# Performance work log

Measured on AMD Instinct MI355X. Metric: run time of the kernel, lower is better.

## Reference

```python
import jax, jax.numpy as jnp
import numpy as np

B, P1, P2 = 32, 25, 24          # batch, patch rows (+1 cls row), patch cols
D1, D2, D3 = 8, 8, 12           # factored embed dims (total d = 768)
H1, H2, H3 = 2, 2, 4            # factored heads (16 total)
X, Y, Z = D1 // H1, D2 // H2, D3 // H3   # per-head factor dims -> head dim 48
SCALE = float((X * Y * Z) ** -0.5)


def tle(x, w1, w2, w3, b):
    # Tensor Linear Embedding: mode-wise linear maps on the last 3 modes + bias.
    return jnp.einsum('bpqijk,ai,cj,dk->bpqacd', x, w1, w2, w3) + b


def split_heads(t):
    # (b,p1,p2,(x h1),(y h2),(z h3)) -> (b,h1,h2,h3, p1*p2, x*y*z)
    b, p1, p2, _, _, _ = t.shape
    t = t.reshape(b, p1, p2, X, H1, Y, H2, Z, H3)
    t = t.transpose(0, 4, 6, 8, 1, 2, 3, 5, 7)
    return t.reshape(b, H1, H2, H3, p1 * p2, X * Y * Z)


def merge_heads(t, p1, p2):
    # (b,h1,h2,h3,S,D) -> (b,p1,p2,(x h1),(y h2),(z h3))
    b = t.shape[0]
    t = t.reshape(b, H1, H2, H3, p1, p2, X, Y, Z)
    t = t.transpose(0, 4, 5, 6, 1, 7, 2, 8, 3)
    return t.reshape(b, p1, p2, X * H1, Y * H2, Z * H3)


def setup_inputs() -> dict:
    key = jax.random.key(0)
    ks = jax.random.split(key, 20)

    def w(k, shape):
        return jax.random.normal(k, shape, jnp.float32) * 0.02

    inp = {"x": jax.random.normal(ks[0], (B, P1, P2, D1, D2, D3), jnp.float32)}
    for i, n in enumerate(["q", "k", "v", "o"]):
        inp[f"w{n}1"] = w(ks[1 + 4 * i], (D1, D1))
        inp[f"w{n}2"] = w(ks[2 + 4 * i], (D2, D2))
        inp[f"w{n}3"] = w(ks[3 + 4 * i], (D3, D3))
        inp[f"b{n}"] = w(ks[4 + 4 * i], (D1, D2, D3))
    return inp


def reference(x, wq1, wq2, wq3, bq, wk1, wk2, wk3, bk,
              wv1, wv2, wv3, bv, wo1, wo2, wo3, bo):
    q = split_heads(tle(x, wq1, wq2, wq3, bq))
    k = split_heads(tle(x, wk1, wk2, wk3, bk))
    v = split_heads(tle(x, wv1, wv2, wv3, bv))
    # scores: (b,h1,h2,h3,S,S) with S = 600
    attn = jax.nn.softmax(jnp.einsum('befgsd,befgtd->befgst', q, k) * SCALE, axis=-1)
    o = jnp.einsum('befgst,befgtd->befgsd', attn, v)
    o = merge_heads(o, P1, P2)
    return tle(o, wo1, wo2, wo3, bo)
```

## Files before the change

### kernel.cpp

```cpp
#include <hip/hip_runtime.h>
#include <hip/hip_bf16.h>
#include <cstdint>

#define Bc    32
#define Sc    600
#define NHc   16
#define SP    640
#define NKT   19
#define DHc   48
#define DP    64
#define QW    48
#define SCALEc 0.14433756729740643f

typedef __bf16   bf16x8 __attribute__((ext_vector_type(8)));
typedef float    f32x4  __attribute__((ext_vector_type(4)));
typedef float    f32x16 __attribute__((ext_vector_type(16)));
typedef uint32_t u32x4  __attribute__((ext_vector_type(4)));

static __device__ __forceinline__ f32x16 mfma32(bf16x8 a, bf16x8 b, f32x16 c) {
    return __builtin_amdgcn_mfma_f32_32x32x16_bf16(a, b, c, 0, 0, 0);
}
static __device__ __forceinline__ unsigned short f2bf(float f) {
    uint32_t u = __builtin_bit_cast(uint32_t, f);
    u += 0x7FFFu + ((u >> 16) & 1u);
    return (unsigned short)(u >> 16);
}
static __device__ __forceinline__ float bfbits(uint32_t w, int odd) {
    return __builtin_bit_cast(float, odd ? (w & 0xffff0000u) : (w << 16));
}
static __device__ __forceinline__ f32x16 fzero16() {
    f32x16 z;
    #pragma unroll
    for (int i = 0; i < 16; ++i) z[i] = 0.f;
    return z;
}
static __device__ __forceinline__ void gload_lds16(const void* g, void* l) {
    __builtin_amdgcn_global_load_lds(
        (const __attribute__((address_space(1))) unsigned int*)g,
        (__attribute__((address_space(3))) unsigned int*)l, 16, 0, 0);
}

__global__ __launch_bounds__(256) void tle_qkv(
    const float* __restrict__ x,
    const float* __restrict__ wq1, const float* __restrict__ wq2,
    const float* __restrict__ wq3, const float* __restrict__ bq,
    const float* __restrict__ wk1, const float* __restrict__ wk2,
    const float* __restrict__ wk3, const float* __restrict__ bk,
    const float* __restrict__ wv1, const float* __restrict__ wv2,
    const float* __restrict__ wv3, const float* __restrict__ bv,
    __hip_bfloat16* __restrict__ Qb, __hip_bfloat16* __restrict__ Kb,
    __hip_bfloat16* __restrict__ Vr)
{
    __shared__ __align__(16) unsigned short t1s[3][4][8][104];
    __shared__ __align__(16) char uni[4*3*16*48*2];
    float (*xs)[768] = (float(*)[768])uni;
    typedef unsigned short outrow_t[3][16][48];
    outrow_t* outs = (outrow_t*)uni;

    const int t = threadIdx.x;
    const int p = t >> 6, a = (t >> 3) & 7, c = t & 7;
    const int patch0 = blockIdx.x * 4;

    {
        const float4* xg = (const float4*)(x + (size_t)patch0 * 768);
        float4* xl = (float4*)uni;
        xl[t] = xg[t]; xl[t + 256] = xg[t + 256]; xl[t + 512] = xg[t + 512];
    }
    float w1r[3][8], w2r[3][8];
    #pragma unroll
    for (int pr = 0; pr < 3; ++pr) {
        const float* w1 = pr == 0 ? wq1 : pr == 1 ? wk1 : wv1;
        const float* w2 = pr == 0 ? wq2 : pr == 1 ? wk2 : wv2;
        #pragma unroll
        for (int i = 0; i < 8; ++i) { w1r[pr][i] = w1[a*8 + i]; w2r[pr][i] = w2[c*8 + i]; }
    }
    __syncthreads();

    float s1[3][12];
    #pragma unroll
    for (int pr = 0; pr < 3; ++pr)
        #pragma unroll
        for (int k = 0; k < 12; ++k) s1[pr][k] = 0.f;
    #pragma unroll
    for (int i = 0; i < 8; ++i) {
        const float4* xr = (const float4*)&xs[p][i*96 + c*12];
        float4 v0 = xr[0], v1 = xr[1], v2 = xr[2];
        #pragma unroll
        for (int pr = 0; pr < 3; ++pr) {
            float wv = w1r[pr][i];
            s1[pr][0] += wv*v0.x; s1[pr][1] += wv*v0.y; s1[pr][2]  += wv*v0.z; s1[pr][3]  += wv*v0.w;
            s1[pr][4] += wv*v1.x; s1[pr][5] += wv*v1.y; s1[pr][6]  += wv*v1.z; s1[pr][7]  += wv*v1.w;
            s1[pr][8] += wv*v2.x; s1[pr][9] += wv*v2.y; s1[pr][10] += wv*v2.z; s1[pr][11] += wv*v2.w;
        }
    }
    #pragma unroll
    for (int pr = 0; pr < 3; ++pr) {
        uint32_t pk[6];
        #pragma unroll
        for (int n = 0; n < 6; ++n)
            asm("v_cvt_pk_bf16_f32 %0, %1, %2" : "=v"(pk[n])
                : "v"(s1[pr][2*n]), "v"(s1[pr][2*n+1]));
        unsigned short* row = &t1s[pr][p][a][0];
        *(uint2*)(row + c*12 + 0) = make_uint2(pk[0], pk[1]);
        *(uint2*)(row + c*12 + 4) = make_uint2(pk[2], pk[3]);
        *(uint2*)(row + c*12 + 8) = make_uint2(pk[4], pk[5]);
    }
    __syncthreads();

    #pragma unroll
    for (int pr = 0; pr < 3; ++pr) {
        uint4 q[12];
        const uint4* t1p = (const uint4*)&t1s[pr][p][a][0];
        #pragma unroll
        for (int n = 0; n < 12; ++n) q[n] = t1p[n];
        float t2r[12];
        #pragma unroll
        for (int k = 0; k < 12; ++k) t2r[k] = 0.f;
        #pragma unroll
        for (int j = 0; j < 8; ++j) {
            float wv = w2r[pr][j];
            #pragma unroll
            for (int k = 0; k < 12; ++k) {
                int idx = j*12 + k;
                uint32_t ww = __builtin_bit_cast(u32x4, q[idx >> 3])[(idx >> 1) & 3];
                t2r[k] += wv * bfbits(ww, idx & 1);
            }
        }
        const float* w3p = pr == 0 ? wq3 : pr == 1 ? wk3 : wv3;
        const float* bb  = pr == 0 ? bq  : pr == 1 ? bk  : bv;
        const float4* bp = (const float4*)(bb + a*96 + c*12);
        float4 b0 = bp[0], b1 = bp[1], b2 = bp[2];
        float bias_[12] = {b0.x,b0.y,b0.z,b0.w, b1.x,b1.y,b1.z,b1.w, b2.x,b2.y,b2.z,b2.w};
        #pragma unroll
        for (int d = 0; d < 12; ++d) {
            const float4* wr = (const float4*)(w3p + d*12);
            float4 u0 = wr[0], u1 = wr[1], u2 = wr[2];
            float od = bias_[d]
                + t2r[0]*u0.x + t2r[1]*u0.y + t2r[2] *u0.z + t2r[3] *u0.w
                + t2r[4]*u1.x + t2r[5]*u1.y + t2r[6] *u1.z + t2r[7] *u1.w
                + t2r[8]*u2.x + t2r[9]*u2.y + t2r[10]*u2.z + t2r[11]*u2.w;
            if (pr == 0) od *= SCALEc;
            int h  = (a & 1)*8 + (c & 1)*4 + (d & 3);
            int dh = (a >> 1)*12 + (c >> 1)*3 + (d >> 2);
            outs[p][pr][h][dh] = f2bf(od);
        }
    }
    __syncthreads();

    #pragma unroll 1
    for (int u = t; u < 1152; u += 256) {
        int pr = u / 384, r = u - pr*384;
        int pp = r / 96,  r2 = r - pp*96;
        int h = r2 / 6,   u6 = r2 - h*6;
        uint4 v = *(const uint4*)&outs[pp][pr][h][u6*8];
        int patch = patch0 + pp;
        int b = patch / Sc, s = patch - b * Sc;
        if (pr == 0)
            *(uint4*)(Qb + ((size_t)(b*NHc + h) * SP + s) * QW + u6*8) = v;
        else if (pr == 1)
            *(uint4*)(Kb + ((size_t)(b*NHc + h) * SP + s) * DP + u6*8) = v;
        else
            *(uint4*)(Vr + ((size_t)(b*NHc + h) * SP + s) * DP + u6*8) = v;
    }
}

__global__ __launch_bounds__(256) void vtrans(
    const __hip_bfloat16* __restrict__ Vr, __hip_bfloat16* __restrict__ Vt,
    __hip_bfloat16* __restrict__ Kb)
{
    __shared__ __align__(16) short Ls[64][72];
    const int t = threadIdx.x;
    const int bh = blockIdx.x, st = blockIdx.y;
    const __hip_bfloat16* src = Vr + ((size_t)bh * SP + st*64) * DP;
    for (int u = t; u < 512; u += 256) {
        int r = u >> 3, c = (u & 7) * 8;
        *(bf16x8*)&Ls[r][c] = *(const bf16x8*)(src + (size_t)r * DP + c);
    }
    __syncthreads();
    const unsigned short one_bf = 0x3F80;
    for (int u = t; u < 384; u += 256) {
        int dh = u >> 3, cb = (u & 7) * 8;
        int gcol = st*64 + cb;
        if (gcol >= Sc + 8) continue;
        union { unsigned short s[8]; bf16x8 v; } o;
        if (gcol >= Sc) {
            #pragma unroll
            for (int j = 0; j < 8; ++j) o.s[j] = 0;
        } else {
            #pragma unroll
            for (int j = 0; j < 8; ++j) o.s[j] = (unsigned short)Ls[cb + j][dh];
        }
        *(bf16x8*)(Vt + ((size_t)bh*64 + dh) * SP + st*64 + cb) = o.v;
    }
    if (t < 128) {
        int r = 48 + (t >> 3), cb = (t & 7) * 8;
        union { unsigned short s[8]; bf16x8 v; } o;
        #pragma unroll
        for (int j = 0; j < 8; ++j) {
            int col = st*64 + cb + j;
            o.s[j] = (r == 48 && col < Sc) ? one_bf : (unsigned short)0;
        }
        *(bf16x8*)(Vt + ((size_t)bh*64 + r) * SP + st*64 + cb) = o.v;
    }
    if (st == 9 && t < 64) {
        int r = 600 + (t >> 3), cb = (t & 7) * 8;
        union { unsigned short s[8]; bf16x8 v; } z;
        #pragma unroll
        for (int j = 0; j < 8; ++j) z.s[j] = 0;
        *(bf16x8*)(Kb + ((size_t)bh * SP + r) * DP + cb) = z.v;
    }
}

static __device__ __forceinline__ void softmax_pack(
    const f32x16& sv, bf16x8& pf0, bf16x8& pf1)
{
    float p[16];
    #pragma unroll
    for (int r = 0; r < 16; ++r) p[r] = __expf(sv[r]);
    uint32_t Wa0, Wa1, Wa2, Wa3, Wb0, Wb1, Wb2, Wb3;
    asm("v_cvt_pk_bf16_f32 %0, %1, %2" : "=v"(Wa0) : "v"(p[0]),  "v"(p[1]));
    asm("v_cvt_pk_bf16_f32 %0, %1, %2" : "=v"(Wb0) : "v"(p[2]),  "v"(p[3]));
    asm("v_cvt_pk_bf16_f32 %0, %1, %2" : "=v"(Wa1) : "v"(p[4]),  "v"(p[5]));
    asm("v_cvt_pk_bf16_f32 %0, %1, %2" : "=v"(Wb1) : "v"(p[6]),  "v"(p[7]));
    asm("v_cvt_pk_bf16_f32 %0, %1, %2" : "=v"(Wa2) : "v"(p[8]),  "v"(p[9]));
    asm("v_cvt_pk_bf16_f32 %0, %1, %2" : "=v"(Wb2) : "v"(p[10]), "v"(p[11]));
    asm("v_cvt_pk_bf16_f32 %0, %1, %2" : "=v"(Wa3) : "v"(p[12]), "v"(p[13]));
    asm("v_cvt_pk_bf16_f32 %0, %1, %2" : "=v"(Wb3) : "v"(p[14]), "v"(p[15]));
    asm("v_permlane32_swap_b32 %0, %1" : "+v"(Wa0), "+v"(Wa1));
    asm("v_permlane32_swap_b32 %0, %1" : "+v"(Wb0), "+v"(Wb1));
    asm("v_permlane32_swap_b32 %0, %1" : "+v"(Wa2), "+v"(Wa3));
    asm("v_permlane32_swap_b32 %0, %1" : "+v"(Wb2), "+v"(Wb3));
    pf0 = __builtin_bit_cast(bf16x8, (u32x4){Wa0, Wb0, Wa1, Wb1});
    pf1 = __builtin_bit_cast(bf16x8, (u32x4){Wa2, Wb2, Wa3, Wb3});
}

__global__ __launch_bounds__(64, 2) void attn_mfma(
    const __hip_bfloat16* __restrict__ Qb, const __hip_bfloat16* __restrict__ Kb,
    const __hip_bfloat16* __restrict__ Vt, float* __restrict__ Ob)
{
    __shared__ __align__(16) char Ks[2][4096];
    __shared__ __align__(16) char Vs[2][4096];
    const int l = threadIdx.x;
    const int q32 = l & 31, hl = l >> 5;
    const int bid = blockIdx.x;
    const int lg = (bid & 7) * 320 + (bid >> 3);
    const int bh = lg / 5, qb = lg - bh * 5;
    const int b = bh >> 4, h = bh & 15;

    const char* Kbh = (const char*)(Kb + (size_t)bh * SP * DP);
    const char* Vbh = (const char*)(Vt + (size_t)bh * 64 * SP);

    const int krow = l >> 3;
    const char* ksrc = Kbh + krow*128 + (((l & 7)*16) ^ (krow << 4));
    const char* vsrc = Vbh + (size_t)(l >> 2)*(SP*2) + (l & 3)*16;

    bf16x8 qf[4][3];
    #pragma unroll
    for (int f = 0; f < 4; ++f) {
        const __hip_bfloat16* Qp = Qb + ((size_t)bh*SP + qb*128 + f*32 + q32) * QW;
        #pragma unroll
        for (int ck = 0; ck < 3; ++ck)
            qf[f][ck] = *(const bf16x8*)(Qp + ck*16 + hl*8);
    }
    f32x16 acc[4][2];
    #pragma unroll
    for (int f = 0; f < 4; ++f) { acc[f][0] = fzero16(); acc[f][1] = fzero16(); }

    auto stage = [&](int kt, int bfi) {
        const char* ks = ksrc + (size_t)kt * 4096;
        const char* vs = vsrc + (size_t)kt * 64;
        #pragma unroll
        for (int i = 0; i < 4; ++i)
            gload_lds16(ks + i*1024, &Ks[bfi][i*1024]);
        #pragma unroll
        for (int i = 0; i < 4; ++i)
            gload_lds16(vs + (size_t)i*16*(SP*2), &Vs[bfi][i*1024]);
    };

    stage(0, 0);
    int bfi = 0;
    #pragma unroll 1
    for (int kt = 0; kt < NKT; ++kt) {
        asm volatile("s_waitcnt vmcnt(0)" ::: "memory");
        __builtin_amdgcn_sched_barrier(0);
        bf16x8 kf[3], vf[2][2];
        #pragma unroll
        for (int ck = 0; ck < 3; ++ck)
            kf[ck] = *(const bf16x8*)&Ks[bfi][q32*128 + ((ck*32 + hl*16) ^ ((q32 & 7) << 4))];
        #pragma unroll
        for (int db = 0; db < 2; ++db)
            #pragma unroll
            for (int c2 = 0; c2 < 2; ++c2)
                vf[db][c2] = *(const bf16x8*)&Vs[bfi][(db*32 + q32)*64 + c2*32 + hl*16];
        if (kt + 1 < NKT) stage(kt + 1, bfi ^ 1);
        __builtin_amdgcn_s_setprio(1);
        #pragma unroll
        for (int f = 0; f < 4; ++f) {
            f32x16 s = fzero16();
            s = mfma32(kf[0], qf[f][0], s);
            s = mfma32(kf[1], qf[f][1], s);
            s = mfma32(kf[2], qf[f][2], s);
            bf16x8 pf0, pf1;
            softmax_pack(s, pf0, pf1);
            acc[f][0] = mfma32(vf[0][0], pf0, acc[f][0]);
            acc[f][0] = mfma32(vf[0][1], pf1, acc[f][0]);
            acc[f][1] = mfma32(vf[1][0], pf0, acc[f][1]);
            acc[f][1] = mfma32(vf[1][1], pf1, acc[f][1]);
        }
        __builtin_amdgcn_s_setprio(0);
        bfi ^= 1;
    }

    #pragma unroll
    for (int f = 0; f < 4; ++f) {
        float ls = acc[f][1][8];
        float other = __shfl_xor(ls, 32);
        float tot = hl ? other : ls;
        float inv = 1.f / tot;
        int q = qb*128 + f*32 + q32;
        if (q < Sc) {
            float* orow = Ob + ((size_t)b*Sc + q)*768 + h*48;
            #pragma unroll
            for (int rq = 0; rq < 4; ++rq) {
                int d0 = rq*8 + hl*4;
                float4 v4 = make_float4(acc[f][0][rq*4+0]*inv, acc[f][0][rq*4+1]*inv,
                                        acc[f][0][rq*4+2]*inv, acc[f][0][rq*4+3]*inv);
                *(float4*)(orow + d0) = v4;
            }
            #pragma unroll
            for (int rq = 0; rq < 2; ++rq) {
                int d0 = 32 + rq*8 + hl*4;
                float4 v4 = make_float4(acc[f][1][rq*4+0]*inv, acc[f][1][rq*4+1]*inv,
                                        acc[f][1][rq*4+2]*inv, acc[f][1][rq*4+3]*inv);
                *(float4*)(orow + d0) = v4;
            }
        }
    }
}

__global__ __launch_bounds__(256) void tle_out(
    const float* __restrict__ Oin, const float* __restrict__ w1g,
    const float* __restrict__ w2g, const float* __restrict__ w3g,
    const float* __restrict__ bias, float* __restrict__ out)
{
    __shared__ __align__(16) float xs[4][768];
    __shared__ __align__(16) unsigned short t1s[4][8][104];
    const int t = threadIdx.x;
    const int p = t >> 6, a = (t >> 3) & 7, c = t & 7;
    const int lane = t & 63;
    const int patch = blockIdx.x * 4 + p;
    for (int o4 = lane; o4 < 192; o4 += 64) {
        float4 v = *(const float4*)(Oin + (size_t)patch * 768 + o4*4);
        int h = o4 / 12, r = o4 - h*12;
        #pragma unroll
        for (int q = 0; q < 4; ++q) {
            int dh = r*4 + q;
            int xq = dh / 12, rem2 = dh - xq*12, yq = rem2 / 3, zq = rem2 - yq*3;
            int aa = xq*2 + (h >> 3), cc = yq*2 + ((h >> 2) & 1), dd = zq*4 + (h & 3);
            xs[p][aa*96 + cc*12 + dd] = ((const float*)&v)[q];
        }
    }
    float w1r[8], w2r[8];
    #pragma unroll
    for (int i = 0; i < 8; ++i) { w1r[i] = w1g[a*8 + i]; w2r[i] = w2g[c*8 + i]; }
    __syncthreads();

    float s1[12];
    #pragma unroll
    for (int k = 0; k < 12; ++k) s1[k] = 0.f;
    #pragma unroll
    for (int i = 0; i < 8; ++i) {
        const float4* xr = (const float4*)&xs[p][i*96 + c*12];
        float4 v0 = xr[0], v1 = xr[1], v2 = xr[2];
        float wv = w1r[i];
        s1[0] += wv*v0.x; s1[1] += wv*v0.y; s1[2]  += wv*v0.z; s1[3]  += wv*v0.w;
        s1[4] += wv*v1.x; s1[5] += wv*v1.y; s1[6]  += wv*v1.z; s1[7]  += wv*v1.w;
        s1[8] += wv*v2.x; s1[9] += wv*v2.y; s1[10] += wv*v2.z; s1[11] += wv*v2.w;
    }
    {
        uint32_t pk[6];
        #pragma unroll
        for (int n = 0; n < 6; ++n)
            asm("v_cvt_pk_bf16_f32 %0, %1, %2" : "=v"(pk[n])
                : "v"(s1[2*n]), "v"(s1[2*n+1]));
        unsigned short* row = &t1s[p][a][0];
        *(uint2*)(row + c*12 + 0) = make_uint2(pk[0], pk[1]);
        *(uint2*)(row + c*12 + 4) = make_uint2(pk[2], pk[3]);
        *(uint2*)(row + c*12 + 8) = make_uint2(pk[4], pk[5]);
    }
    __syncthreads();

    uint4 q[12];
    const uint4* t1p = (const uint4*)&t1s[p][a][0];
    #pragma unroll
    for (int n = 0; n < 12; ++n) q[n] = t1p[n];
    float t2r[12];
    #pragma unroll
    for (int k = 0; k < 12; ++k) t2r[k] = 0.f;
    #pragma unroll
    for (int j = 0; j < 8; ++j) {
        float wv = w2r[j];
        #pragma unroll
        for (int k = 0; k < 12; ++k) {
            int idx = j*12 + k;
            uint32_t ww = __builtin_bit_cast(u32x4, q[idx >> 3])[(idx >> 1) & 3];
            t2r[k] += wv * bfbits(ww, idx & 1);
        }
    }
    const float4* bp = (const float4*)(bias + a*96 + c*12);
    float4 b0 = bp[0], b1 = bp[1], b2 = bp[2];
    float bias_[12] = {b0.x,b0.y,b0.z,b0.w, b1.x,b1.y,b1.z,b1.w, b2.x,b2.y,b2.z,b2.w};
    float od[12];
    #pragma unroll
    for (int d = 0; d < 12; ++d) {
        const float4* wr = (const float4*)(w3g + d*12);
        float4 u0 = wr[0], u1 = wr[1], u2 = wr[2];
        od[d] = bias_[d]
            + t2r[0]*u0.x + t2r[1]*u0.y + t2r[2] *u0.z + t2r[3] *u0.w
            + t2r[4]*u1.x + t2r[5]*u1.y + t2r[6] *u1.z + t2r[7] *u1.w
            + t2r[8]*u2.x + t2r[9]*u2.y + t2r[10]*u2.z + t2r[11]*u2.w;
    }
    float4* op = (float4*)(out + (size_t)patch*768 + a*96 + c*12);
    op[0] = make_float4(od[0], od[1], od[2],  od[3]);
    op[1] = make_float4(od[4], od[5], od[6],  od[7]);
    op[2] = make_float4(od[8], od[9], od[10], od[11]);
}

extern "C" void kernel_launch(void* const* d_in, const int* in_sizes, int n_in,
                              void* d_out, int out_size, void* d_ws, size_t ws_size,
                              hipStream_t stream) {
    const float* x   = (const float*)d_in[0];
    const float* wq1 = (const float*)d_in[1];
    const float* wq2 = (const float*)d_in[2];
    const float* wq3 = (const float*)d_in[3];
    const float* bq  = (const float*)d_in[4];
    const float* wk1 = (const float*)d_in[5];
    const float* wk2 = (const float*)d_in[6];
    const float* wk3 = (const float*)d_in[7];
    const float* bk  = (const float*)d_in[8];
    const float* wv1 = (const float*)d_in[9];
    const float* wv2 = (const float*)d_in[10];
    const float* wv3 = (const float*)d_in[11];
    const float* bv  = (const float*)d_in[12];
    const float* wo1 = (const float*)d_in[13];
    const float* wo2 = (const float*)d_in[14];
    const float* wo3 = (const float*)d_in[15];
    const float* bo  = (const float*)d_in[16];
    float* out = (float*)d_out;

    char* ws = (char*)d_ws;
    const size_t SZ_Q = (size_t)512 * SP * QW * 2;
    const size_t SZ_K = (size_t)512 * SP * DP * 2;
    __hip_bfloat16* Qb = (__hip_bfloat16*)ws;
    __hip_bfloat16* Kb = (__hip_bfloat16*)(ws + SZ_Q);
    __hip_bfloat16* Vr = (__hip_bfloat16*)(ws + SZ_Q + SZ_K);
    __hip_bfloat16* Vt = (__hip_bfloat16*)(ws + SZ_Q + 2*SZ_K);
    float*          Ob = (float*)(ws + SZ_Q + 3*SZ_K);

    dim3 blk(256);
    tle_qkv<<<Bc*Sc/4, blk, 0, stream>>>(x, wq1, wq2, wq3, bq,
                                         wk1, wk2, wk3, bk,
                                         wv1, wv2, wv3, bv, Qb, Kb, Vr);
    vtrans<<<dim3(512, 10), blk, 0, stream>>>(Vr, Vt, Kb);
    attn_mfma<<<2560, 64, 0, stream>>>(Qb, Kb, Vt, Ob);
    tle_out<<<Bc*Sc/4, blk, 0, stream>>>(Ob, wo1, wo2, wo3, bo, out);
}
```

Baseline: 178.6 us.

## Rewrite QKV tensor embedding with MFMA Kronecker-factored first stage and fp16 dot2

The QKV projection kernel now processes 16 patches per block. The first two mode products are fused into one GEMM by forming the Kronecker product of w1 and w2 in bf16 and running it on 16x16x32 MFMA instructions. The third mode uses packed fp16 dot2 instructions on an fp16 intermediate held in LDS, and each thread writes one full contiguous head row directly to global memory. This replaces scalar FMA loops and a separate LDS transpose-and-store pass, at the cost of lower intermediate precision (bf16 weights product, fp16 intermediate) and a serial loop over the three projections with barriers.

```diff
diff --git a/kernel.cpp b/kernel.cpp
--- a/kernel.cpp
+++ b/kernel.cpp
@@ -12,21 +12,21 @@
 #define QW    48
 #define SCALEc 0.14433756729740643f
 
-typedef __bf16   bf16x8 __attribute__((ext_vector_type(8)));
-typedef float    f32x4  __attribute__((ext_vector_type(4)));
-typedef float    f32x16 __attribute__((ext_vector_type(16)));
-typedef uint32_t u32x4  __attribute__((ext_vector_type(4)));
-
+typedef __bf16    bf16x8 __attribute__((ext_vector_type(8)));
+typedef float     f32x4  __attribute__((ext_vector_type(4)));
+typedef float     f32x16 __attribute__((ext_vector_type(16)));
+typedef uint32_t  u32x4  __attribute__((ext_vector_type(4)));
+typedef _Float16  f16x2  __attribute__((ext_vector_type(2)));
+
+static __device__ __forceinline__ f32x4 mfma16(bf16x8 a, bf16x8 b, f32x4 c) {
+    return __builtin_amdgcn_mfma_f32_16x16x32_bf16(a, b, c, 0, 0, 0);
+}
 static __device__ __forceinline__ f32x16 mfma32(bf16x8 a, bf16x8 b, f32x16 c) {
     return __builtin_amdgcn_mfma_f32_32x32x16_bf16(a, b, c, 0, 0, 0);
 }
-static __device__ __forceinline__ unsigned short f2bf(float f) {
-    uint32_t u = __builtin_bit_cast(uint32_t, f);
-    u += 0x7FFFu + ((u >> 16) & 1u);
-    return (unsigned short)(u >> 16);
-}
-static __device__ __forceinline__ float bfbits(uint32_t w, int odd) {
-    return __builtin_bit_cast(float, odd ? (w & 0xffff0000u) : (w << 16));
+static __device__ __forceinline__ float fdot2u(uint32_t a, uint32_t b, float c) {
+    return __builtin_amdgcn_fdot2(__builtin_bit_cast(f16x2, a),
+                                  __builtin_bit_cast(f16x2, b), c, false);
 }
 static __device__ __forceinline__ f32x16 fzero16() {
     f32x16 z;
@@ -40,7 +40,7 @@
         (__attribute__((address_space(3))) unsigned int*)l, 16, 0, 0);
 }
 
-__global__ __launch_bounds__(256) void tle_qkv(
+__global__ __launch_bounds__(256, 3) void tle_qkv(
     const float* __restrict__ x,
     const float* __restrict__ wq1, const float* __restrict__ wq2,
     const float* __restrict__ wq3, const float* __restrict__ bq,
@@ -51,116 +51,150 @@
     __hip_bfloat16* __restrict__ Qb, __hip_bfloat16* __restrict__ Kb,
     __hip_bfloat16* __restrict__ Vr)
 {
-    __shared__ __align__(16) unsigned short t1s[3][4][8][104];
-    __shared__ __align__(16) char uni[4*3*16*48*2];
-    float (*xs)[768] = (float(*)[768])uni;
-    typedef unsigned short outrow_t[3][16][48];
-    outrow_t* outs = (outrow_t*)uni;
-
+    __shared__ __align__(16) unsigned short xb[16*864];
+    __shared__ __align__(16) unsigned short t2s[16*776];
     const int t = threadIdx.x;
-    const int p = t >> 6, a = (t >> 3) & 7, c = t & 7;
-    const int patch0 = blockIdx.x * 4;
+    const int patch0 = blockIdx.x * 16;
 
     {
-        const float4* xg = (const float4*)(x + (size_t)patch0 * 768);
-        float4* xl = (float4*)uni;
-        xl[t] = xg[t]; xl[t + 256] = xg[t + 256]; xl[t + 512] = xg[t + 512];
-    }
-    float w1r[3][8], w2r[3][8];
-    #pragma unroll
+        const int pl = t >> 4, ij0 = (t & 15) * 4;
+        const float4* xg = (const float4*)(x + (size_t)(patch0 + pl) * 768 + ij0*12);
+        float vv[4][12];
+        #pragma unroll
+        for (int ij = 0; ij < 4; ++ij) {
+            float4 a = xg[ij*3+0], b = xg[ij*3+1], c = xg[ij*3+2];
+            vv[ij][0]=a.x; vv[ij][1]=a.y; vv[ij][2]=a.z;  vv[ij][3]=a.w;
+            vv[ij][4]=b.x; vv[ij][5]=b.y; vv[ij][6]=b.z;  vv[ij][7]=b.w;
+            vv[ij][8]=c.x; vv[ij][9]=c.y; vv[ij][10]=c.z; vv[ij][11]=c.w;
+        }
+        #pragma unroll
+        for (int k = 0; k < 12; ++k) {
+            uint32_t lo, hi;
+            asm("v_cvt_pk_bf16_f32 %0, %1, %2" : "=v"(lo) : "v"(vv[0][k]), "v"(vv[1][k]));
+            asm("v_cvt_pk_bf16_f32 %0, %1, %2" : "=v"(hi) : "v"(vv[2][k]), "v"(vv[3][k]));
+            *(uint2*)&xb[pl*864 + k*72 + ij0] = make_uint2(lo, hi);
+        }
+    }
+    __syncthreads();
+
+    const int l = t & 63, w = t >> 6;
+    const int r16 = l & 15, g = l >> 4;
+
+    bf16x8 Bf[3][2];
+    int pl_c[3], k_c[3];
+    #pragma unroll
+    for (int n = 0; n < 3; ++n) {
+        int col = n*16 + r16;
+        int pp = col / 12, kk = col - pp*12;
+        pl_c[n] = w*4 + pp; k_c[n] = kk;
+        #pragma unroll
+        for (int kh = 0; kh < 2; ++kh)
+            Bf[n][kh] = *(const bf16x8*)&xb[pl_c[n]*864 + kk*72 + kh*32 + g*8];
+    }
+
+    const int plo = t >> 4, h = t & 15;
+    const int h1 = h >> 3, h2 = (h >> 2) & 1, h3 = h & 3;
+    const int patch3 = patch0 + plo;
+    const int b3 = patch3 / Sc, s3 = patch3 - b3*Sc;
+
+    #pragma unroll 1
     for (int pr = 0; pr < 3; ++pr) {
         const float* w1 = pr == 0 ? wq1 : pr == 1 ? wk1 : wv1;
         const float* w2 = pr == 0 ? wq2 : pr == 1 ? wk2 : wv2;
-        #pragma unroll
-        for (int i = 0; i < 8; ++i) { w1r[pr][i] = w1[a*8 + i]; w2r[pr][i] = w2[c*8 + i]; }
-    }
-    __syncthreads();
-
-    float s1[3][12];
-    #pragma unroll
-    for (int pr = 0; pr < 3; ++pr)
-        #pragma unroll
-        for (int k = 0; k < 12; ++k) s1[pr][k] = 0.f;
-    #pragma unroll
-    for (int i = 0; i < 8; ++i) {
-        const float4* xr = (const float4*)&xs[p][i*96 + c*12];
-        float4 v0 = xr[0], v1 = xr[1], v2 = xr[2];
-        #pragma unroll
-        for (int pr = 0; pr < 3; ++pr) {
-            float wv = w1r[pr][i];
-            s1[pr][0] += wv*v0.x; s1[pr][1] += wv*v0.y; s1[pr][2]  += wv*v0.z; s1[pr][3]  += wv*v0.w;
-            s1[pr][4] += wv*v1.x; s1[pr][5] += wv*v1.y; s1[pr][6]  += wv*v1.z; s1[pr][7]  += wv*v1.w;
-            s1[pr][8] += wv*v2.x; s1[pr][9] += wv*v2.y; s1[pr][10] += wv*v2.z; s1[pr][11] += wv*v2.w;
-        }
-    }
-    #pragma unroll
-    for (int pr = 0; pr < 3; ++pr) {
-        uint32_t pk[6];
-        #pragma unroll
-        for (int n = 0; n < 6; ++n)
-            asm("v_cvt_pk_bf16_f32 %0, %1, %2" : "=v"(pk[n])
-                : "v"(s1[pr][2*n]), "v"(s1[pr][2*n+1]));
-        unsigned short* row = &t1s[pr][p][a][0];
-        *(uint2*)(row + c*12 + 0) = make_uint2(pk[0], pk[1]);
-        *(uint2*)(row + c*12 + 4) = make_uint2(pk[2], pk[3]);
-        *(uint2*)(row + c*12 + 8) = make_uint2(pk[4], pk[5]);
-    }
-    __syncthreads();
-
-    #pragma unroll
-    for (int pr = 0; pr < 3; ++pr) {
-        uint4 q[12];
-        const uint4* t1p = (const uint4*)&t1s[pr][p][a][0];
-        #pragma unroll
-        for (int n = 0; n < 12; ++n) q[n] = t1p[n];
-        float t2r[12];
-        #pragma unroll
-        for (int k = 0; k < 12; ++k) t2r[k] = 0.f;
-        #pragma unroll
-        for (int j = 0; j < 8; ++j) {
-            float wv = w2r[pr][j];
-            #pragma unroll
-            for (int k = 0; k < 12; ++k) {
-                int idx = j*12 + k;
-                uint32_t ww = __builtin_bit_cast(u32x4, q[idx >> 3])[(idx >> 1) & 3];
-                t2r[k] += wv * bfbits(ww, idx & 1);
+        float w2r[8];
+        #pragma unroll
+        for (int j = 0; j < 8; ++j) w2r[j] = w2[(r16 & 7)*8 + j];
+        bf16x8 Af[4][2];
+        #pragma unroll
+        for (int m = 0; m < 4; ++m) {
+            int a = 2*m + (r16 >> 3);
+            #pragma unroll
+            for (int kh = 0; kh < 2; ++kh) {
+                float w1v = w1[a*8 + kh*4 + g];
+                uint32_t wd[4];
+                #pragma unroll
+                for (int q = 0; q < 4; ++q)
+                    asm("v_cvt_pk_bf16_f32 %0, %1, %2" : "=v"(wd[q])
+                        : "v"(w1v*w2r[2*q]), "v"(w1v*w2r[2*q+1]));
+                Af[m][kh] = __builtin_bit_cast(bf16x8, (u32x4){wd[0],wd[1],wd[2],wd[3]});
             }
         }
-        const float* w3p = pr == 0 ? wq3 : pr == 1 ? wk3 : wv3;
-        const float* bb  = pr == 0 ? bq  : pr == 1 ? bk  : bv;
-        const float4* bp = (const float4*)(bb + a*96 + c*12);
-        float4 b0 = bp[0], b1 = bp[1], b2 = bp[2];
-        float bias_[12] = {b0.x,b0.y,b0.z,b0.w, b1.x,b1.y,b1.z,b1.w, b2.x,b2.y,b2.z,b2.w};
-        #pragma unroll
-        for (int d = 0; d < 12; ++d) {
-            const float4* wr = (const float4*)(w3p + d*12);
-            float4 u0 = wr[0], u1 = wr[1], u2 = wr[2];
-            float od = bias_[d]
-                + t2r[0]*u0.x + t2r[1]*u0.y + t2r[2] *u0.z + t2r[3] *u0.w
-                + t2r[4]*u1.x + t2r[5]*u1.y + t2r[6] *u1.z + t2r[7] *u1.w
-                + t2r[8]*u2.x + t2r[9]*u2.y + t2r[10]*u2.z + t2r[11]*u2.w;
-            if (pr == 0) od *= SCALEc;
-            int h  = (a & 1)*8 + (c & 1)*4 + (d & 3);
-            int dh = (a >> 1)*12 + (c >> 1)*3 + (d >> 2);
-            outs[p][pr][h][dh] = f2bf(od);
-        }
-    }
-    __syncthreads();
-
-    #pragma unroll 1
-    for (int u = t; u < 1152; u += 256) {
-        int pr = u / 384, r = u - pr*384;
-        int pp = r / 96,  r2 = r - pp*96;
-        int h = r2 / 6,   u6 = r2 - h*6;
-        uint4 v = *(const uint4*)&outs[pp][pr][h][u6*8];
-        int patch = patch0 + pp;
-        int b = patch / Sc, s = patch - b * Sc;
-        if (pr == 0)
-            *(uint4*)(Qb + ((size_t)(b*NHc + h) * SP + s) * QW + u6*8) = v;
-        else if (pr == 1)
-            *(uint4*)(Kb + ((size_t)(b*NHc + h) * SP + s) * DP + u6*8) = v;
-        else
-            *(uint4*)(Vr + ((size_t)(b*NHc + h) * SP + s) * DP + u6*8) = v;
+        f32x4 acc[4][3];
+        #pragma unroll
+        for (int m = 0; m < 4; ++m)
+            #pragma unroll
+            for (int n = 0; n < 3; ++n) acc[m][n] = f32x4{0.f,0.f,0.f,0.f};
+        #pragma unroll
+        for (int m = 0; m < 4; ++m)
+            #pragma unroll
+            for (int n = 0; n < 3; ++n) {
+                acc[m][n] = mfma16(Af[m][0], Bf[n][0], acc[m][n]);
+                acc[m][n] = mfma16(Af[m][1], Bf[n][1], acc[m][n]);
+            }
+        #pragma unroll
+        for (int m = 0; m < 4; ++m)
+            #pragma unroll
+            for (int n = 0; n < 3; ++n)
+                #pragma unroll
+                for (int r = 0; r < 4; ++r) {
+                    int ac = m*16 + g*4 + r;
+                    _Float16 hv = (_Float16)acc[m][n][r];
+                    t2s[pl_c[n]*776 + ac*12 + k_c[n]] =
+                        __builtin_bit_cast(unsigned short, hv);
+                }
+        __syncthreads();
+
+        const float* w3 = pr == 0 ? wq3 : pr == 1 ? wk3 : wv3;
+        const float* bb = pr == 0 ? bq  : pr == 1 ? bk  : bv;
+        uint32_t w3p[3][6];
+        #pragma unroll
+        for (int z = 0; z < 3; ++z) {
+            const float* wr = w3 + (z*4 + h3)*12;
+            #pragma unroll
+            for (int q = 0; q < 6; ++q)
+                w3p[z][q] = __builtin_bit_cast(uint32_t,
+                    __builtin_amdgcn_cvt_pkrtz(wr[2*q], wr[2*q+1]));
+        }
+        float od[48];
+        #pragma unroll
+        for (int xq = 0; xq < 4; ++xq)
+            #pragma unroll
+            for (int yq = 0; yq < 4; ++yq) {
+                int a = xq*2 + h1, c = yq*2 + h2;
+                int ac = a*8 + c;
+                const uint2* tp = (const uint2*)&t2s[plo*776 + ac*12];
+                uint2 q0 = tp[0], q1 = tp[1], q2 = tp[2];
+                const float* bp = bb + a*96 + c*12 + h3;
+                #pragma unroll
+                for (int z = 0; z < 3; ++z) {
+                    float a3 = bp[z*4];
+                    a3 = fdot2u(q0.x, w3p[z][0], a3);
+                    a3 = fdot2u(q0.y, w3p[z][1], a3);
+                    a3 = fdot2u(q1.x, w3p[z][2], a3);
+                    a3 = fdot2u(q1.y, w3p[z][3], a3);
+                    a3 = fdot2u(q2.x, w3p[z][4], a3);
+                    a3 = fdot2u(q2.y, w3p[z][5], a3);
+                    od[xq*12 + yq*3 + z] = a3;
+                }
+            }
+        if (pr == 0) {
+            #pragma unroll
+            for (int i2 = 0; i2 < 48; ++i2) od[i2] *= SCALEc;
+        }
+        __hip_bfloat16* dst = pr == 0 ? Qb : pr == 1 ? Kb : Vr;
+        const int pitch = pr == 0 ? QW : DP;
+        unsigned short* drow = (unsigned short*)dst
+            + ((size_t)(b3*NHc + h) * SP + s3) * pitch;
+        #pragma unroll
+        for (int u = 0; u < 6; ++u) {
+            uint32_t wd[4];
+            #pragma unroll
+            for (int q = 0; q < 4; ++q)
+                asm("v_cvt_pk_bf16_f32 %0, %1, %2" : "=v"(wd[q])
+                    : "v"(od[u*8 + 2*q]), "v"(od[u*8 + 2*q + 1]));
+            *(uint4*)(drow + u*8) = make_uint4(wd[0], wd[1], wd[2], wd[3]);
+        }
+        __syncthreads();
     }
 }
 
@@ -404,7 +438,9 @@
         for (int k = 0; k < 12; ++k) {
             int idx = j*12 + k;
             uint32_t ww = __builtin_bit_cast(u32x4, q[idx >> 3])[(idx >> 1) & 3];
-            t2r[k] += wv * bfbits(ww, idx & 1);
+            float xv = __builtin_bit_cast(float,
+                (idx & 1) ? (ww & 0xffff0000u) : (ww << 16));
+            t2r[k] += wv * xv;
         }
     }
     const float4* bp = (const float4*)(bias + a*96 + c*12);
@@ -457,11 +493,10 @@
     __hip_bfloat16* Vt = (__hip_bfloat16*)(ws + SZ_Q + 2*SZ_K);
     float*          Ob = (float*)(ws + SZ_Q + 3*SZ_K);
 
-    dim3 blk(256);
-    tle_qkv<<<Bc*Sc/4, blk, 0, stream>>>(x, wq1, wq2, wq3, bq,
-                                         wk1, wk2, wk3, bk,
-                                         wv1, wv2, wv3, bv, Qb, Kb, Vr);
-    vtrans<<<dim3(512, 10), blk, 0, stream>>>(Vr, Vt, Kb);
+    tle_qkv<<<Bc*Sc/16, 256, 0, stream>>>(x, wq1, wq2, wq3, bq,
+                                          wk1, wk2, wk3, bk,
+                                          wv1, wv2, wv3, bv, Qb, Kb, Vr);
+    vtrans<<<dim3(512, 10), 256, 0, stream>>>(Vr, Vt, Kb);
     attn_mfma<<<2560, 64, 0, stream>>>(Qb, Kb, Vt, Ob);
-    tle_out<<<Bc*Sc/4, blk, 0, stream>>>(Ob, wo1, wo2, wo3, bo, out);
-}
+    tle_out<<<Bc*Sc/4, 256, 0, stream>>>(Ob, wo1, wo2, wo3, bo, out);
+}
```

Result: faster. 166.9 us (-6.5%).
